# Kernel optimization log

Hardware: AMD Instinct MI355X
Metric: run time of the kernel (lower is better)

Reference implementation:

```python
import jax, jax.numpy as jnp
import numpy as np
import math

DIM = 1024
THETA = 10000.0


def rope_cos_sin(seq_len, dim, dtype=jnp.float32):
    # freqs over pairs: 1/theta^(2i/dim), angles = t * freq
    inv = 1.0 / (THETA ** (jnp.arange(0, dim, 2, dtype=jnp.float32) / dim))  # [dim/2]
    t = jnp.arange(seq_len, dtype=jnp.float32)
    ang = jnp.outer(t, inv)  # [S, dim/2]
    return jnp.cos(ang).astype(dtype), jnp.sin(ang).astype(dtype)


def apply_rotary(x, cos, sin):
    # x: [B, S, D]; treat consecutive pairs as complex (xr + i*xi)
    B, S, D = x.shape
    xr = x[..., 0::2]  # [B, S, D/2]
    xi = x[..., 1::2]
    or_ = xr * cos - xi * sin
    oi_ = xr * sin + xi * cos
    # interleave back: (..., D/2, 2) -> (..., D)
    return jnp.stack([or_, oi_], axis=-1).reshape(B, S, D)


def setup_inputs() -> dict:
    key = jax.random.key(0)
    ks = jax.random.split(key, 5)
    B, S, D = 4, 2048, DIM
    x = jax.random.normal(ks[0], (B, S, D), dtype=jnp.float32)
    s = 1.0 / math.sqrt(D)
    wq = jax.random.normal(ks[1], (D, D), dtype=jnp.float32) * s
    wk = jax.random.normal(ks[2], (D, D), dtype=jnp.float32) * s
    wv = jax.random.normal(ks[3], (D, D), dtype=jnp.float32) * s
    wo = jax.random.normal(ks[4], (D, D), dtype=jnp.float32) * s
    return {"x": x, "wq": wq, "wk": wk, "wv": wv, "wo": wo}


def reference(x, wq, wk, wv, wo):
    B, S, D = x.shape
    xq = jnp.einsum('bsd,ed->bse', x, wq)  # Linear: x @ W^T
    xk = jnp.einsum('bsd,ed->bse', x, wk)
    xv = jnp.einsum('bsd,ed->bse', x, wv)
    cos, sin = rope_cos_sin(S, D, x.dtype)
    xq = apply_rotary(xq, cos, sin)
    xk = apply_rotary(xk, cos, sin)
    scores = jnp.einsum('bqd,bkd->bqk', xq, xk) / jnp.sqrt(jnp.asarray(D, x.dtype))
    attn = jax.nn.softmax(scores, axis=-1)  # no causal mask in original
    out = jnp.einsum('bqk,bkd->bqd', attn, xv)
    return jnp.einsum('bsd,ed->bse', out, wo)
```

## Files before the change

### kernel.cpp

```cpp
#include <hip/hip_runtime.h>
#include <math.h>

typedef __attribute__((ext_vector_type(8))) short short8;
typedef __attribute__((ext_vector_type(4))) float f32x4;
typedef unsigned short u16;

__device__ __forceinline__ float b2f(u16 u) {
    union { unsigned u; float f; } c; c.u = ((unsigned)u) << 16; return c.f;
}
__device__ __forceinline__ u16 f2b(float f) {
    unsigned u = __float_as_uint(f);
    u += 0x7fffu + ((u >> 16) & 1u);
    return (u16)(u >> 16);
}

__device__ __forceinline__ void gl_lds16(const u16* g, u16* l) {
    __builtin_amdgcn_global_load_lds(
        (const __attribute__((address_space(1))) void*)g,
        (__attribute__((address_space(3))) void*)l,
        16, 0, 0);
}

__global__ __launch_bounds__(256) void cvt_f32_bf16(const float* __restrict__ src,
                                                    u16* __restrict__ dst, int n) {
    const int i = (blockIdx.x * 256 + threadIdx.x) * 8;
    if (i >= n) return;
    const float4 a = *(const float4*)&src[i];
    const float4 b = *(const float4*)&src[i + 4];
    short8 o;
    o[0] = (short)f2b(a.x); o[1] = (short)f2b(a.y);
    o[2] = (short)f2b(a.z); o[3] = (short)f2b(a.w);
    o[4] = (short)f2b(b.x); o[5] = (short)f2b(b.y);
    o[6] = (short)f2b(b.z); o[7] = (short)f2b(b.w);
    *(short8*)&dst[i] = o;
}

__global__ __launch_bounds__(256) void cvt_weights(
    const float* __restrict__ w0, const float* __restrict__ w1,
    const float* __restrict__ w2, const float* __restrict__ w3,
    u16* __restrict__ dst) {
    const int z = blockIdx.z;
    const float* src = (z == 0) ? w0 : (z == 1) ? w1 : (z == 2) ? w2 : w3;
    const int i = (blockIdx.x * 256 + threadIdx.x) * 8;
    const float4 a = *(const float4*)&src[i];
    const float4 b = *(const float4*)&src[i + 4];
    short8 o;
    o[0] = (short)f2b(a.x); o[1] = (short)f2b(a.y);
    o[2] = (short)f2b(a.z); o[3] = (short)f2b(a.w);
    o[4] = (short)f2b(b.x); o[5] = (short)f2b(b.y);
    o[6] = (short)f2b(b.z); o[7] = (short)f2b(b.w);
    *(short8*)&dst[(long)z * 1024 * 1024 + i] = o;
}

template<typename OT>
__device__ __forceinline__ void gemm256_body(
    const u16* __restrict__ A, const u16* __restrict__ W, OT* __restrict__ C,
    int lda, int ldw, int ldc, int K, float scale)
{
    __shared__ u16 lsA[4 * 8192];
    __shared__ u16 lsB[4 * 8192];

    const int m0 = blockIdx.y * 256;
    const int n0 = blockIdx.x * 256;
    const int t = threadIdx.x;
    const int lane = t & 63;
    const int w = t >> 6;
    const int wm = (w & 1) * 128;
    const int wn = (w >> 1) * 64;
    const int fr = lane & 15;
    const int fq = lane >> 4;

    const int srow = t >> 2;
    const int scol = ((t & 3) ^ ((t >> 3) & 3)) * 8;
    const u16* pA0 = A + (long)(m0 + srow) * lda + scol;
    const u16* pA1 = A + (long)(m0 + 128 + srow) * lda + scol;
    const u16* pW0 = W + (long)(n0 + srow) * ldw + scol;
    const u16* pW1 = W + (long)(n0 + 128 + srow) * ldw + scol;
    const int tld = t * 8;

    f32x4 acc[8][4];
#pragma unroll
    for (int i = 0; i < 8; ++i)
#pragma unroll
        for (int j = 0; j < 4; ++j)
            acc[i][j] = (f32x4){0.f, 0.f, 0.f, 0.f};

    const int swz = (fq ^ ((fr >> 1) & 3)) * 8;
    const int aoff = (wm + fr) * 32 + swz;
    const int boff = (wn + fr) * 32 + swz;

#define STAGE256(s) do { \
    const int _sl = ((s) & 3) * 8192; const int _ko = (s) * 32; \
    gl_lds16(pA0 + _ko, &lsA[_sl + tld]); \
    gl_lds16(pA1 + _ko, &lsA[_sl + 4096 + tld]); \
    gl_lds16(pW0 + _ko, &lsB[_sl + tld]); \
    gl_lds16(pW1 + _ko, &lsB[_sl + 4096 + tld]); \
} while (0)

    const int n2 = K >> 5;

    STAGE256(0);
    STAGE256(1);
    STAGE256(2);
    asm volatile("s_waitcnt vmcnt(8)" ::: "memory");
    __builtin_amdgcn_sched_barrier(0);
    __builtin_amdgcn_s_barrier();
    __builtin_amdgcn_sched_barrier(0);

    for (int st = 0; st < n2; ++st) {
        const int slot = (st & 3) * 8192;
        short8 af[8], bfr[4];
        af[0] = *(const short8*)&lsA[slot + aoff];
#pragma unroll
        for (int n = 0; n < 4; ++n)
            bfr[n] = *(const short8*)&lsB[slot + boff + n * 512];
#pragma unroll
        for (int m = 1; m < 8; ++m)
            af[m] = *(const short8*)&lsA[slot + aoff + m * 512];

        if (st + 3 < n2) {
            STAGE256(st + 3);
            asm volatile("s_waitcnt vmcnt(8)" ::: "memory");
        } else if (st + 2 < n2) {
            asm volatile("s_waitcnt vmcnt(4)" ::: "memory");
        } else if (st + 1 < n2) {
            asm volatile("s_waitcnt vmcnt(0)" ::: "memory");
        }

        __builtin_amdgcn_s_setprio(1);
#pragma unroll
        for (int m = 0; m < 8; ++m)
#pragma unroll
            for (int n = 0; n < 4; ++n)
                acc[m][n] = __builtin_amdgcn_mfma_f32_16x16x32_bf16(
                    af[m], bfr[n], acc[m][n], 0, 0, 0);
        __builtin_amdgcn_s_setprio(0);

        __builtin_amdgcn_sched_barrier(0);
        __builtin_amdgcn_s_barrier();
        __builtin_amdgcn_sched_barrier(0);
    }
#undef STAGE256

#pragma unroll
    for (int m = 0; m < 8; ++m) {
        const int row0 = m0 + wm + m * 16 + fq * 4;
#pragma unroll
        for (int n = 0; n < 4; ++n) {
            const int col = n0 + wn + n * 16 + fr;
#pragma unroll
            for (int r = 0; r < 4; ++r) {
                const float val = acc[m][n][r] * scale;
                if (sizeof(OT) == 2) {
                    ((u16*)C)[(long)(row0 + r) * ldc + col] = f2b(val);
                } else {
                    ((float*)C)[(long)(row0 + r) * ldc + col] = val;
                }
            }
        }
    }
}

template<typename OT>
__global__ __launch_bounds__(512, 2) void gemm256_bt(
    const u16* __restrict__ A, const u16* __restrict__ W, OT* __restrict__ C,
    int lda, int ldw, int ldc, int K,
    long sA, long sW, long sC, float scale)
{
    const int z = blockIdx.z;
    gemm256_body<OT>(A + (long)z * sA, W + (long)z * sW, C + (long)z * sC,
                     lda, ldw, ldc, K, scale);
}

__global__ __launch_bounds__(512, 2) void gemm256_dual(
    const u16* __restrict__ A0, const u16* __restrict__ W0, u16* __restrict__ C0,
    int lda0, int ldw0, int ldc0, long sA0, long sW0, long sC0, float scale0,
    const u16* __restrict__ A1, const u16* __restrict__ W1, u16* __restrict__ C1,
    int lda1, int ldw1, int ldc1, long sA1, long sW1, long sC1, float scale1)
{
    const int z = blockIdx.z;
    const u16 *A, *W; u16 *C; int lda, ldw, ldc; float scl;
    if (z < 4) {
        A = A0 + (long)z * sA0; W = W0 + (long)z * sW0; C = C0 + (long)z * sC0;
        lda = lda0; ldw = ldw0; ldc = ldc0; scl = scale0;
    } else {
        if (blockIdx.y >= 4) return;
        const int b = z - 4;
        A = A1 + (long)b * sA1; W = W1 + (long)b * sW1; C = C1 + (long)b * sC1;
        lda = lda1; ldw = ldw1; ldc = ldc1; scl = scale1;
    }
    gemm256_body<u16>(A, W, C, lda, ldw, ldc, 1024, scl);
}

template<typename OT>
__device__ __forceinline__ void gemm_body(
    const u16* __restrict__ A, const u16* __restrict__ W, OT* __restrict__ C,
    int lda, int ldw, int ldc, int K, float scale)
{
    __shared__ u16 lsA[2][128 * 32];
    __shared__ u16 lsB[2][128 * 32];

    const int m0 = blockIdx.y * 128;
    const int n0 = blockIdx.x * 128;
    const int t = threadIdx.x;
    const int lane = t & 63;
    const int wave = t >> 6;
    const int wm = (wave & 1) * 64;
    const int wn = (wave >> 1) * 64;

    const int sr = t >> 2;
    const int scol = ((t & 3) ^ ((t >> 3) & 3)) * 8;

    const u16* pa0 = A + (long)(m0 + sr) * lda + scol;
    const u16* pa1 = pa0 + (long)64 * lda;
    const u16* pw0 = W + (long)(n0 + sr) * ldw + scol;
    const u16* pw1 = pw0 + (long)64 * ldw;

    f32x4 acc[4][4];
#pragma unroll
    for (int i = 0; i < 4; ++i)
#pragma unroll
        for (int j = 0; j < 4; ++j)
            acc[i][j] = (f32x4){0.f, 0.f, 0.f, 0.f};

    const int fr = lane & 15;
    const int fq = lane >> 4;
    const int swz = (fq ^ ((fr >> 1) & 3)) * 8;
    const int aoff = (wm + fr) * 32 + swz;
    const int boff = (wn + fr) * 32 + swz;

    gl_lds16(pa0, &lsA[0][t * 8]);        pa0 += 32;
    gl_lds16(pa1, &lsA[0][2048 + t * 8]); pa1 += 32;
    gl_lds16(pw0, &lsB[0][t * 8]);        pw0 += 32;
    gl_lds16(pw1, &lsB[0][2048 + t * 8]); pw1 += 32;

    const int nsteps = K >> 5;
    int par = 0;
    for (int s = 0; s < nsteps; ++s) {
        __syncthreads();
        if (s + 1 < nsteps) {
            const int np = par ^ 1;
            gl_lds16(pa0, &lsA[np][t * 8]);        pa0 += 32;
            gl_lds16(pa1, &lsA[np][2048 + t * 8]); pa1 += 32;
            gl_lds16(pw0, &lsB[np][t * 8]);        pw0 += 32;
            gl_lds16(pw1, &lsB[np][2048 + t * 8]); pw1 += 32;
        }

        short8 af[4], bf[4];
#pragma unroll
        for (int i = 0; i < 4; ++i)
            af[i] = *(const short8*)&lsA[par][aoff + i * 512];
#pragma unroll
        for (int j = 0; j < 4; ++j)
            bf[j] = *(const short8*)&lsB[par][boff + j * 512];
#pragma unroll
        for (int i = 0; i < 4; ++i)
#pragma unroll
            for (int j = 0; j < 4; ++j)
                acc[i][j] = __builtin_amdgcn_mfma_f32_16x16x32_bf16(af[i], bf[j], acc[i][j], 0, 0, 0);
        par ^= 1;
    }

#pragma unroll
    for (int i = 0; i < 4; ++i) {
#pragma unroll
        for (int j = 0; j < 4; ++j) {
            const int row0 = m0 + wm + i * 16 + fq * 4;
            const int col = n0 + wn + j * 16 + fr;
#pragma unroll
            for (int r = 0; r < 4; ++r) {
                const int row = row0 + r;
                const float val = acc[i][j][r] * scale;
                if (sizeof(OT) == 2) {
                    ((u16*)C)[(long)row * ldc + col] = f2b(val);
                } else {
                    ((float*)C)[(long)row * ldc + col] = val;
                }
            }
        }
    }
}

template<typename OT>
__global__ __launch_bounds__(256) void gemm_bt(
    const u16* __restrict__ A, const u16* __restrict__ W, OT* __restrict__ C,
    int lda, int ldw, int ldc, int K,
    long sA, long sW, long sC, float scale)
{
    const int bz = blockIdx.z;
    gemm_body<OT>(A + (long)bz * sA, W + (long)bz * sW, C + (long)bz * sC,
                  lda, ldw, ldc, K, scale);
}

__global__ __launch_bounds__(256) void rope_kernel(u16* q, u16* k) {
    const int row = blockIdx.x;
    const int pos = row & 2047;
    u16* p = (blockIdx.y ? k : q) + (long)row * 1024;
#pragma unroll
    for (int it = 0; it < 2; ++it) {
        const int i = threadIdx.x + it * 256;
        const float e = (float)i * (1.0f / 512.0f);
        const float inv = powf(10000.0f, -e);
        const float ang = (float)pos * inv;
        float s, c;
        sincosf(ang, &s, &c);
        const float xr = b2f(p[2 * i]);
        const float xi = b2f(p[2 * i + 1]);
        p[2 * i]     = f2b(xr * c - xi * s);
        p[2 * i + 1] = f2b(xr * s + xi * c);
    }
}

__global__ __launch_bounds__(256) void softmax_kernel(const u16* __restrict__ S, u16* __restrict__ P) {
    const long row = blockIdx.x;
    const u16* src = S + row * 2048;
    u16* dst = P + row * 2048;
    const int t = threadIdx.x;
    const int lane = t & 63;
    const int wave = t >> 6;
    __shared__ float red[4];

    float v[8];
    const short8 raw = *(const short8*)&src[t * 8];
#pragma unroll
    for (int i = 0; i < 8; ++i) v[i] = b2f((u16)raw[i]);

    float m = v[0];
#pragma unroll
    for (int i = 1; i < 8; ++i) m = fmaxf(m, v[i]);
    for (int o = 32; o > 0; o >>= 1) m = fmaxf(m, __shfl_xor(m, o, 64));
    if (lane == 0) red[wave] = m;
    __syncthreads();
    m = fmaxf(fmaxf(red[0], red[1]), fmaxf(red[2], red[3]));
    __syncthreads();

    float sum = 0.f;
#pragma unroll
    for (int i = 0; i < 8; ++i) { v[i] = expf(v[i] - m); sum += v[i]; }
    for (int o = 32; o > 0; o >>= 1) sum += __shfl_xor(sum, o, 64);
    if (lane == 0) red[wave] = sum;
    __syncthreads();
    sum = red[0] + red[1] + red[2] + red[3];
    const float is = 1.0f / sum;

    short8 outv;
#pragma unroll
    for (int i = 0; i < 8; ++i) outv[i] = (short)f2b(v[i] * is);
    *(short8*)&dst[t * 8] = outv;
}

extern "C" void kernel_launch(void* const* d_in, const int* in_sizes, int n_in,
                              void* d_out, int out_size, void* d_ws, size_t ws_size,
                              hipStream_t stream)
{
    (void)in_sizes; (void)n_in; (void)out_size; (void)ws_size;
    const float* x  = (const float*)d_in[0];
    const float* wq = (const float*)d_in[1];
    const float* wk = (const float*)d_in[2];
    const float* wv = (const float*)d_in[3];
    const float* wo = (const float*)d_in[4];
    float* out = (float*)d_out;

    const long M1 = 1024 * 1024;
    u16* ws  = (u16*)d_ws;
    u16* xb  = ws;
    u16* wqb = xb + 8 * M1;
    u16* wob = wqb + 3 * M1;
    u16* q   = wqb + 4 * M1;
    u16* kk  = q + 8 * M1;
    u16* v   = kk + 8 * M1;
    u16* sc  = v + 8 * M1;
    u16* UT  = xb;

    const dim3 blk(256);
    const dim3 blk5(512);

    cvt_f32_bf16<<<dim3(4096), blk, 0, stream>>>(x, xb, 8 * 1024 * 1024);
    cvt_weights<<<dim3(512, 1, 4), blk, 0, stream>>>(wq, wk, wv, wo, wqb);

    gemm256_bt<u16><<<dim3(4, 32, 3), blk5, 0, stream>>>(xb, wqb, q,
        1024, 1024, 1024, 1024, 0, M1, 8 * M1, 1.0f);

    rope_kernel<<<dim3(8192, 2), blk, 0, stream>>>(q, kk);

    gemm256_dual<<<dim3(8, 8, 8), blk5, 0, stream>>>(
        q, kk, sc, 1024, 1024, 2048, 2 * M1, 2 * M1, 4 * M1, 0.03125f,
        wob, v, UT, 1024, 1024, 2048, 0, 2 * M1, 2 * M1, 1.0f);

    softmax_kernel<<<dim3(8192), blk, 0, stream>>>(sc, sc);

    gemm_bt<float><<<dim3(8, 16, 4), blk, 0, stream>>>(sc, UT, out,
        2048, 2048, 1024, 2048, 4 * M1, 2 * M1, 2 * M1, 1.0f);
}
```

Measured before the change: 339.1 us.

## Double-buffer register fragments and interleave LDS reads with MFMA halves in GEMMs

Both GEMM bodies now keep two register fragment sets and read the next stage's A/B fragments from LDS between the two halves of the current stage's MFMAs. This hides LDS read latency behind matrix math. The 128-tile GEMM also moves from a 2-slot to a 4-slot global-to-LDS ring with 3-stage prefetch, and gemm_bt gains a launch-bounds occupancy hint of 2. The extra fragment registers and larger LDS footprint could reduce occupancy, and the loop unrolled by two assumes an even step count.

```diff
diff --git a/kernel.cpp b/kernel.cpp
--- a/kernel.cpp
+++ b/kernel.cpp
@@ -52,6 +52,29 @@
     *(short8*)&dst[(long)z * 1024 * 1024 + i] = o;
 }
 
+template<int MLO>
+__device__ __forceinline__ void mfma_half256(f32x4 (&acc)[8][4],
+                                             const short8 (&AF)[8],
+                                             const short8 (&BF)[4]) {
+#pragma unroll
+    for (int m = 0; m < 4; ++m)
+#pragma unroll
+        for (int n = 0; n < 4; ++n)
+            acc[MLO + m][n] = __builtin_amdgcn_mfma_f32_16x16x32_bf16(
+                AF[MLO + m], BF[n], acc[MLO + m][n], 0, 0, 0);
+}
+template<int MLO>
+__device__ __forceinline__ void mfma_half128(f32x4 (&acc)[4][4],
+                                             const short8 (&AF)[4],
+                                             const short8 (&BF)[4]) {
+#pragma unroll
+    for (int m = 0; m < 2; ++m)
+#pragma unroll
+        for (int n = 0; n < 4; ++n)
+            acc[MLO + m][n] = __builtin_amdgcn_mfma_f32_16x16x32_bf16(
+                AF[MLO + m], BF[n], acc[MLO + m][n], 0, 0, 0);
+}
+
 template<typename OT>
 __device__ __forceinline__ void gemm256_body(
     const u16* __restrict__ A, const u16* __restrict__ W, OT* __restrict__ C,
@@ -97,49 +120,57 @@
     gl_lds16(pW1 + _ko, &lsB[_sl + 4096 + tld]); \
 } while (0)
 
+#define READS256(s, AF, BF) do { \
+    const int _sl = ((s) & 3) * 8192; \
+    _Pragma("unroll") \
+    for (int _n = 0; _n < 4; ++_n) \
+        BF[_n] = *(const short8*)&lsB[_sl + boff + _n * 512]; \
+    _Pragma("unroll") \
+    for (int _m = 0; _m < 8; ++_m) \
+        AF[_m] = *(const short8*)&lsA[_sl + aoff + _m * 512]; \
+} while (0)
+
+#define PHASE256(stv, CA, CB, NA, NB) do { \
+    const int _st = (stv); \
+    if (_st + 3 < n2) STAGE256(_st + 3); \
+    __builtin_amdgcn_sched_barrier(0); \
+    __builtin_amdgcn_s_setprio(1); \
+    mfma_half256<0>(acc, CA, CB); \
+    __builtin_amdgcn_s_setprio(0); \
+    __builtin_amdgcn_sched_barrier(0); \
+    if (_st + 1 < n2) READS256(_st + 1, NA, NB); \
+    __builtin_amdgcn_sched_barrier(0); \
+    __builtin_amdgcn_s_setprio(1); \
+    mfma_half256<4>(acc, CA, CB); \
+    __builtin_amdgcn_s_setprio(0); \
+    if (_st + 3 < n2) { asm volatile("s_waitcnt vmcnt(4)" ::: "memory"); } \
+    else if (_st + 2 < n2) { asm volatile("s_waitcnt vmcnt(0)" ::: "memory"); } \
+    if (_st + 1 < n2) { \
+        __builtin_amdgcn_sched_barrier(0); \
+        __builtin_amdgcn_s_barrier(); \
+        __builtin_amdgcn_sched_barrier(0); \
+    } \
+} while (0)
+
     const int n2 = K >> 5;
+
+    short8 a0[8], b0[4], a1[8], b1[4];
 
     STAGE256(0);
     STAGE256(1);
     STAGE256(2);
-    asm volatile("s_waitcnt vmcnt(8)" ::: "memory");
+    asm volatile("s_waitcnt vmcnt(4)" ::: "memory");
     __builtin_amdgcn_sched_barrier(0);
     __builtin_amdgcn_s_barrier();
     __builtin_amdgcn_sched_barrier(0);
-
-    for (int st = 0; st < n2; ++st) {
-        const int slot = (st & 3) * 8192;
-        short8 af[8], bfr[4];
-        af[0] = *(const short8*)&lsA[slot + aoff];
-#pragma unroll
-        for (int n = 0; n < 4; ++n)
-            bfr[n] = *(const short8*)&lsB[slot + boff + n * 512];
-#pragma unroll
-        for (int m = 1; m < 8; ++m)
-            af[m] = *(const short8*)&lsA[slot + aoff + m * 512];
-
-        if (st + 3 < n2) {
-            STAGE256(st + 3);
-            asm volatile("s_waitcnt vmcnt(8)" ::: "memory");
-        } else if (st + 2 < n2) {
-            asm volatile("s_waitcnt vmcnt(4)" ::: "memory");
-        } else if (st + 1 < n2) {
-            asm volatile("s_waitcnt vmcnt(0)" ::: "memory");
-        }
-
-        __builtin_amdgcn_s_setprio(1);
-#pragma unroll
-        for (int m = 0; m < 8; ++m)
-#pragma unroll
-            for (int n = 0; n < 4; ++n)
-                acc[m][n] = __builtin_amdgcn_mfma_f32_16x16x32_bf16(
-                    af[m], bfr[n], acc[m][n], 0, 0, 0);
-        __builtin_amdgcn_s_setprio(0);
-
-        __builtin_amdgcn_sched_barrier(0);
-        __builtin_amdgcn_s_barrier();
-        __builtin_amdgcn_sched_barrier(0);
-    }
+    READS256(0, a0, b0);
+
+    for (int st = 0; st < n2; st += 2) {
+        PHASE256(st,     a0, b0, a1, b1);
+        PHASE256(st + 1, a1, b1, a0, b0);
+    }
+#undef PHASE256
+#undef READS256
 #undef STAGE256
 
 #pragma unroll
@@ -197,8 +228,8 @@
     const u16* __restrict__ A, const u16* __restrict__ W, OT* __restrict__ C,
     int lda, int ldw, int ldc, int K, float scale)
 {
-    __shared__ u16 lsA[2][128 * 32];
-    __shared__ u16 lsB[2][128 * 32];
+    __shared__ u16 lsA[4 * 4096];
+    __shared__ u16 lsB[4 * 4096];
 
     const int m0 = blockIdx.y * 128;
     const int n0 = blockIdx.x * 128;
@@ -212,9 +243,10 @@
     const int scol = ((t & 3) ^ ((t >> 3) & 3)) * 8;
 
     const u16* pa0 = A + (long)(m0 + sr) * lda + scol;
-    const u16* pa1 = pa0 + (long)64 * lda;
+    const u16* pa1 = A + (long)(m0 + 64 + sr) * lda + scol;
     const u16* pw0 = W + (long)(n0 + sr) * ldw + scol;
-    const u16* pw1 = pw0 + (long)64 * ldw;
+    const u16* pw1 = W + (long)(n0 + 64 + sr) * ldw + scol;
+    const int tld = t * 8;
 
     f32x4 acc[4][4];
 #pragma unroll
@@ -229,37 +261,66 @@
     const int aoff = (wm + fr) * 32 + swz;
     const int boff = (wn + fr) * 32 + swz;
 
-    gl_lds16(pa0, &lsA[0][t * 8]);        pa0 += 32;
-    gl_lds16(pa1, &lsA[0][2048 + t * 8]); pa1 += 32;
-    gl_lds16(pw0, &lsB[0][t * 8]);        pw0 += 32;
-    gl_lds16(pw1, &lsB[0][2048 + t * 8]); pw1 += 32;
-
-    const int nsteps = K >> 5;
-    int par = 0;
-    for (int s = 0; s < nsteps; ++s) {
-        __syncthreads();
-        if (s + 1 < nsteps) {
-            const int np = par ^ 1;
-            gl_lds16(pa0, &lsA[np][t * 8]);        pa0 += 32;
-            gl_lds16(pa1, &lsA[np][2048 + t * 8]); pa1 += 32;
-            gl_lds16(pw0, &lsB[np][t * 8]);        pw0 += 32;
-            gl_lds16(pw1, &lsB[np][2048 + t * 8]); pw1 += 32;
-        }
-
-        short8 af[4], bf[4];
-#pragma unroll
-        for (int i = 0; i < 4; ++i)
-            af[i] = *(const short8*)&lsA[par][aoff + i * 512];
-#pragma unroll
-        for (int j = 0; j < 4; ++j)
-            bf[j] = *(const short8*)&lsB[par][boff + j * 512];
-#pragma unroll
-        for (int i = 0; i < 4; ++i)
-#pragma unroll
-            for (int j = 0; j < 4; ++j)
-                acc[i][j] = __builtin_amdgcn_mfma_f32_16x16x32_bf16(af[i], bf[j], acc[i][j], 0, 0, 0);
-        par ^= 1;
-    }
+#define STAGE128(s) do { \
+    const int _sl = ((s) & 3) * 4096; const int _ko = (s) * 32; \
+    gl_lds16(pa0 + _ko, &lsA[_sl + tld]); \
+    gl_lds16(pa1 + _ko, &lsA[_sl + 2048 + tld]); \
+    gl_lds16(pw0 + _ko, &lsB[_sl + tld]); \
+    gl_lds16(pw1 + _ko, &lsB[_sl + 2048 + tld]); \
+} while (0)
+
+#define READS128(s, AF, BF) do { \
+    const int _sl = ((s) & 3) * 4096; \
+    _Pragma("unroll") \
+    for (int _n = 0; _n < 4; ++_n) \
+        BF[_n] = *(const short8*)&lsB[_sl + boff + _n * 512]; \
+    _Pragma("unroll") \
+    for (int _m = 0; _m < 4; ++_m) \
+        AF[_m] = *(const short8*)&lsA[_sl + aoff + _m * 512]; \
+} while (0)
+
+#define PHASE128(stv, CA, CB, NA, NB) do { \
+    const int _st = (stv); \
+    if (_st + 3 < n2) STAGE128(_st + 3); \
+    __builtin_amdgcn_sched_barrier(0); \
+    __builtin_amdgcn_s_setprio(1); \
+    mfma_half128<0>(acc, CA, CB); \
+    __builtin_amdgcn_s_setprio(0); \
+    __builtin_amdgcn_sched_barrier(0); \
+    if (_st + 1 < n2) READS128(_st + 1, NA, NB); \
+    __builtin_amdgcn_sched_barrier(0); \
+    __builtin_amdgcn_s_setprio(1); \
+    mfma_half128<2>(acc, CA, CB); \
+    __builtin_amdgcn_s_setprio(0); \
+    if (_st + 3 < n2) { asm volatile("s_waitcnt vmcnt(4)" ::: "memory"); } \
+    else if (_st + 2 < n2) { asm volatile("s_waitcnt vmcnt(0)" ::: "memory"); } \
+    if (_st + 1 < n2) { \
+        __builtin_amdgcn_sched_barrier(0); \
+        __builtin_amdgcn_s_barrier(); \
+        __builtin_amdgcn_sched_barrier(0); \
+    } \
+} while (0)
+
+    const int n2 = K >> 5;
+
+    short8 a0[4], b0[4], a1[4], b1[4];
+
+    STAGE128(0);
+    STAGE128(1);
+    STAGE128(2);
+    asm volatile("s_waitcnt vmcnt(4)" ::: "memory");
+    __builtin_amdgcn_sched_barrier(0);
+    __builtin_amdgcn_s_barrier();
+    __builtin_amdgcn_sched_barrier(0);
+    READS128(0, a0, b0);
+
+    for (int st = 0; st < n2; st += 2) {
+        PHASE128(st,     a0, b0, a1, b1);
+        PHASE128(st + 1, a1, b1, a0, b0);
+    }
+#undef PHASE128
+#undef READS128
+#undef STAGE128
 
 #pragma unroll
     for (int i = 0; i < 4; ++i) {
@@ -282,7 +343,7 @@
 }
 
 template<typename OT>
-__global__ __launch_bounds__(256) void gemm_bt(
+__global__ __launch_bounds__(256, 2) void gemm_bt(
     const u16* __restrict__ A, const u16* __restrict__ W, OT* __restrict__ C,
     int lda, int ldw, int ldc, int K,
     long sA, long sW, long sC, float scale)
```

Result: slower. 346.2 us (+2.1%).
